# Kernel optimization log

Measured on AMD Instinct MI355X. Metric: run time of the kernel, lower is better.

## Reference

```python
import jax, jax.numpy as jnp
import numpy as np
import math

K_HEADS = 16  # nb_heads from init_kwargs


def setup_inputs() -> dict:
    key = jax.random.key(0)
    ks = jax.random.split(key, 7)
    B, M, H, D = 2, 2048, 1024, 1024 // K_HEADS
    return {
        "h": jax.random.normal(ks[0], (B, M, H), jnp.float32),
        "h_cache": jax.random.normal(ks[1], (B, M, H), jnp.float32),
        "key_pe": jax.random.normal(ks[2], (1, D, M), jnp.float32),
        "Wq": jax.random.normal(ks[3], (H, H), jnp.float32) * 0.02,
        "Wk": jax.random.normal(ks[4], (H, H), jnp.float32) * 0.02,
        "Wv": jax.random.normal(ks[5], (H, H), jnp.float32) * 0.02,
        "Wo": jax.random.normal(ks[6], (H, H), jnp.float32) * 0.02,
    }


def _heads(x, K):
    # [B, M, H] -> [B, K, M, D]
    B, M, H = x.shape
    return x.reshape(B, M, K, H // K).transpose(0, 2, 1, 3)


def reference(h, h_cache, key_pe, Wq, Wk, Wv, Wo):
    B, M, H = h.shape
    K = K_HEADS
    D = H // K
    q = _heads(h @ Wq.T, K)        # [B, K, M, D]
    k = _heads(h_cache @ Wk.T, K)  # [B, K, L, D], L == M
    v = _heads(h_cache @ Wv.T, K)  # [B, K, L, D]

    attn_cont = jnp.einsum("bkmd,bkld->bkml", q, k)            # content scores
    attn_pos = jnp.einsum("bkmd,dl->bkml", q, key_pe[0])       # positional scores
    attn = (attn_cont + attn_pos[..., :M]) / math.sqrt(D)
    attn = jax.nn.softmax(attn, axis=-1)  # computed as in source, but source
    # (faithfully) multiplies VALUE by attn_cont, not attn:
    out = jnp.einsum("bkml,bkld->bkmd", attn_cont, v)          # [B, K, M, D]
    out = out.transpose(0, 2, 1, 3).reshape(B, M, H)
    return out @ Wo.T
```

## Files before the change

kernel.cpp:

```cpp
#include <hip/hip_runtime.h>
#include <hip/hip_bf16.h>

#define BB 2
#define MM 2048
#define HH 1024
#define KH 16

typedef short s16x8 __attribute__((ext_vector_type(8)));
typedef float f32x4 __attribute__((ext_vector_type(4)));
typedef float f32x16 __attribute__((ext_vector_type(16)));

#define GLOBAL_AS __attribute__((address_space(1)))
#define LDS_AS    __attribute__((address_space(3)))

__device__ __forceinline__ void async_copy16(const void* g, void* l) {
    __builtin_amdgcn_global_load_lds((const GLOBAL_AS void*)g, (LDS_AS void*)l, 16, 0, 0);
}

struct __align__(8) bf16x4_t { __hip_bfloat16 x, y, z, w; };

__global__ __launch_bounds__(256) void cvt6b(
    const float* __restrict__ s0, const float* __restrict__ s1,
    const float* __restrict__ s2, const float* __restrict__ s3,
    const float* __restrict__ s4,
    __hip_bfloat16* __restrict__ d0, __hip_bfloat16* __restrict__ d1,
    __hip_bfloat16* __restrict__ d2, __hip_bfloat16* __restrict__ d3,
    __hip_bfloat16* __restrict__ d4,
    float* __restrict__ Sz)
{
    const int seg = blockIdx.y;
    const int i = (blockIdx.x * 256 + threadIdx.x) * 4;
    if (seg == 5) {
        if (i + 3 < BB * KH * 64 * 64) {
            float4 z = {0.f, 0.f, 0.f, 0.f};
            *(float4*)(Sz + i) = z;
        }
        return;
    }
    const float* src;
    __hip_bfloat16* dst;
    int n;
    switch (seg) {
        case 0: src = s0; dst = d0; n = BB * MM * HH; break;
        case 1: src = s1; dst = d1; n = BB * MM * HH; break;
        case 2: src = s2; dst = d2; n = HH * HH; break;
        case 3: src = s3; dst = d3; n = HH * HH; break;
        default: src = s4; dst = d4; n = HH * HH; break;
    }
    if (i + 3 < n) {
        const float4 v = *(const float4*)(src + i);
        bf16x4_t o;
        o.x = __float2bfloat16(v.x);
        o.y = __float2bfloat16(v.y);
        o.z = __float2bfloat16(v.z);
        o.w = __float2bfloat16(v.w);
        *(bf16x4_t*)(dst + i) = o;
    }
}

__global__ __launch_bounds__(256) void transpose_wq(
    const float* __restrict__ Wq, __hip_bfloat16* __restrict__ WqT)
{
    __shared__ float Tl[64][65];
    const int j0 = blockIdx.x * 64;
    const int k0 = blockIdx.y * 64;
    const int t = threadIdx.x;
    const int r = t >> 6;
    const int c = t & 63;
#pragma unroll
    for (int i = 0; i < 64; i += 4)
        Tl[r + i][c] = Wq[(size_t)(j0 + r + i) * HH + k0 + c];
    __syncthreads();
#pragma unroll
    for (int i = 0; i < 64; i += 4)
        WqT[(size_t)(k0 + r + i) * HH + j0 + c] = __float2bfloat16(Tl[c][r + i]);
}

__device__ __forceinline__ void store_c(__hip_bfloat16* C, size_t idx, float v) {
    C[idx] = __float2bfloat16(v);
}
__device__ __forceinline__ void store_c(float* C, size_t idx, float v) { C[idx] = v; }

template <typename OutT>
__device__ __forceinline__ void gemm_nt_body64(
    const __hip_bfloat16* __restrict__ A,
    const __hip_bfloat16* __restrict__ Bm,
    OutT* __restrict__ C,
    __hip_bfloat16* As, __hip_bfloat16* Bs,
    int m0, int n0)
{
    const int t    = threadIdx.x;
    const int lane = t & 63;
    const int wave = t >> 6;

    const int srow = lane >> 3;
    const int sw   = ((lane & 7) ^ srow) * 8;

    const int wm  = (wave >> 1) * 64;
    const int wn  = (wave & 1) * 64;
    const int fm  = lane & 31;
    const int fm7 = fm & 7;
    const int ghi = lane >> 5;

    f32x16 acc[2][2] = {};

    for (int k0 = 0; k0 < HH; k0 += 64) {
        __syncthreads();
#pragma unroll
        for (int i = 0; i < 2; ++i) {
            const int c = wave * 2 + i;
            const __hip_bfloat16* ag = A + (size_t)(m0 + c * 16 + srow) * HH + k0 + sw;
            async_copy16(ag,          As + c * 1024);
            async_copy16(ag + 8 * HH, As + c * 1024 + 512);
            const __hip_bfloat16* bg = Bm + (size_t)(n0 + c * 16 + srow) * HH + k0 + sw;
            async_copy16(bg,          Bs + c * 1024);
            async_copy16(bg + 8 * HH, Bs + c * 1024 + 512);
        }
        __syncthreads();

#pragma unroll
        for (int ks = 0; ks < 64; ks += 16) {
            const int pos = ((((ks >> 3) + ghi) ^ fm7) * 8);
            s16x8 af[2], bf[2];
#pragma unroll
            for (int mi = 0; mi < 2; ++mi)
                af[mi] = *(const s16x8*)(As + (wm + mi * 32 + fm) * 64 + pos);
#pragma unroll
            for (int ni = 0; ni < 2; ++ni)
                bf[ni] = *(const s16x8*)(Bs + (wn + ni * 32 + fm) * 64 + pos);
#pragma unroll
            for (int mi = 0; mi < 2; ++mi)
#pragma unroll
                for (int ni = 0; ni < 2; ++ni)
                    acc[mi][ni] = __builtin_amdgcn_mfma_f32_32x32x16_bf16(
                        af[mi], bf[ni], acc[mi][ni], 0, 0, 0);
        }
    }

    const int ec = lane & 31;
    const int eb = (lane >> 5) * 4;
#pragma unroll
    for (int mi = 0; mi < 2; ++mi)
#pragma unroll
        for (int ni = 0; ni < 2; ++ni)
#pragma unroll
            for (int r = 0; r < 16; ++r) {
                const int m = m0 + wm + mi * 32 + (r & 3) + 8 * (r >> 2) + eb;
                const int n = n0 + wn + ni * 32 + ec;
                store_c(C, (size_t)m * HH + n, acc[mi][ni][r]);
            }
}

template <typename OutT>
__device__ __forceinline__ void gemm_nt_body64_m64(
    const __hip_bfloat16* __restrict__ A,
    const __hip_bfloat16* __restrict__ Bm,
    OutT* __restrict__ C,
    __hip_bfloat16* As, __hip_bfloat16* Bs,
    int m0, int n0)
{
    const int t    = threadIdx.x;
    const int lane = t & 63;
    const int wave = t >> 6;

    const int srow = lane >> 3;
    const int sw   = ((lane & 7) ^ srow) * 8;

    const int wn  = wave * 32;
    const int fm  = lane & 31;
    const int fm7 = fm & 7;
    const int ghi = lane >> 5;

    f32x16 acc[2] = {};

    for (int k0 = 0; k0 < HH; k0 += 64) {
        __syncthreads();
        {
            const __hip_bfloat16* ag = A + (size_t)(m0 + wave * 16 + srow) * HH + k0 + sw;
            async_copy16(ag,          As + wave * 1024);
            async_copy16(ag + 8 * HH, As + wave * 1024 + 512);
        }
#pragma unroll
        for (int i = 0; i < 2; ++i) {
            const int c = wave * 2 + i;
            const __hip_bfloat16* bg = Bm + (size_t)(n0 + c * 16 + srow) * HH + k0 + sw;
            async_copy16(bg,          Bs + c * 1024);
            async_copy16(bg + 8 * HH, Bs + c * 1024 + 512);
        }
        __syncthreads();

#pragma unroll
        for (int ks = 0; ks < 64; ks += 16) {
            const int pos = ((((ks >> 3) + ghi) ^ fm7) * 8);
            s16x8 af[2], bf;
#pragma unroll
            for (int mi = 0; mi < 2; ++mi)
                af[mi] = *(const s16x8*)(As + (mi * 32 + fm) * 64 + pos);
            bf = *(const s16x8*)(Bs + (wn + fm) * 64 + pos);
#pragma unroll
            for (int mi = 0; mi < 2; ++mi)
                acc[mi] = __builtin_amdgcn_mfma_f32_32x32x16_bf16(
                    af[mi], bf, acc[mi], 0, 0, 0);
        }
    }

    const int ec = lane & 31;
    const int eb = (lane >> 5) * 4;
#pragma unroll
    for (int mi = 0; mi < 2; ++mi)
#pragma unroll
        for (int r = 0; r < 16; ++r) {
            const int m = m0 + mi * 32 + (r & 3) + 8 * (r >> 2) + eb;
            const int n = n0 + wn + ec;
            store_c(C, (size_t)m * HH + n, acc[mi][r]);
        }
}

__global__ __launch_bounds__(256) void gemm_kv(
    const __hip_bfloat16* __restrict__ hcb,
    const __hip_bfloat16* __restrict__ wk, const __hip_bfloat16* __restrict__ wv,
    __hip_bfloat16* __restrict__ K, __hip_bfloat16* __restrict__ V)
{
    __shared__ __align__(16) __hip_bfloat16 As[128 * 64];
    __shared__ __align__(16) __hip_bfloat16 Bs[128 * 64];
    const int z = blockIdx.z;
    gemm_nt_body64(hcb, z ? wv : wk, z ? V : K, As, Bs,
                   blockIdx.x * 128, blockIdx.y * 128);
}

__global__ __launch_bounds__(256) void gemm_f(
    const __hip_bfloat16* __restrict__ W2, const __hip_bfloat16* __restrict__ WqT,
    __hip_bfloat16* __restrict__ F)
{
    __shared__ __align__(16) __hip_bfloat16 As[64 * 64];
    __shared__ __align__(16) __hip_bfloat16 Bs[128 * 64];
    const int b = blockIdx.z;
    gemm_nt_body64_m64(W2 + (size_t)b * HH * HH, WqT, F + (size_t)b * HH * HH,
                       As, Bs, blockIdx.x * 64, blockIdx.y * 128);
}

__global__ __launch_bounds__(256) void gemm_final(
    const __hip_bfloat16* __restrict__ hb, const __hip_bfloat16* __restrict__ F,
    float* __restrict__ outg)
{
    __shared__ __align__(16) __hip_bfloat16 As[64 * 64];
    __shared__ __align__(16) __hip_bfloat16 Bs[128 * 64];
    const int b = blockIdx.z;
    gemm_nt_body64_m64(hb + (size_t)b * MM * HH, F + (size_t)b * HH * HH,
                       outg + (size_t)b * MM * HH, As, Bs,
                       blockIdx.x * 64, blockIdx.y * 128);
}

#define CH 128
#define LP 136

__global__ __launch_bounds__(256) void kv_outer_mfma(
    const __hip_bfloat16* __restrict__ Km,
    const __hip_bfloat16* __restrict__ Vm,
    float* __restrict__ S)
{
    __shared__ __align__(16) __hip_bfloat16 Kt[64 * LP];
    __shared__ __align__(16) __hip_bfloat16 Vt[64 * LP];

    const int t = threadIdx.x, head = blockIdx.y, b = blockIdx.z;
    const int l0 = blockIdx.x * CH;

    const int r  = t & 127;
    const int cb = (t >> 7) * 8;
    const size_t gbase = (size_t)(b * MM + l0 + r) * HH + head * 64;
#pragma unroll
    for (int u = 0; u < 4; ++u) {
        const int c8 = cb + u * 16;
        const s16x8 kv = *(const s16x8*)(Km + gbase + c8);
        const s16x8 vv = *(const s16x8*)(Vm + gbase + c8);
#pragma unroll
        for (int j = 0; j < 8; ++j) {
            Kt[(c8 + j) * LP + r] = ((const __hip_bfloat16*)&kv)[j];
            Vt[(c8 + j) * LP + r] = ((const __hip_bfloat16*)&vv)[j];
        }
    }
    __syncthreads();

    const int wave = t >> 6, lane = t & 63;
    const int fr = lane & 15;
    const int fq = (lane >> 4) * 8;
    const int wm = wave * 16;

    f32x4 acc[4] = {};
    for (int kk = 0; kk < CH; kk += 32) {
        const s16x8 af = *(const s16x8*)(Kt + (wm + fr) * LP + kk + fq);
        s16x8 bf[4];
#pragma unroll
        for (int nj = 0; nj < 4; ++nj)
            bf[nj] = *(const s16x8*)(Vt + (nj * 16 + fr) * LP + kk + fq);
#pragma unroll
        for (int nj = 0; nj < 4; ++nj)
            acc[nj] = __builtin_amdgcn_mfma_f32_16x16x32_bf16(af, bf[nj], acc[nj], 0, 0, 0);
    }

    float* Sg = S + ((size_t)b * KH + head) * 4096;
    const int er = (lane >> 4) * 4;
    const int ec = lane & 15;
#pragma unroll
    for (int nj = 0; nj < 4; ++nj)
#pragma unroll
        for (int rr = 0; rr < 4; ++rr)
            atomicAdd(&Sg[(wm + er + rr) * 64 + nj * 16 + ec], acc[nj][rr]);
}

__global__ __launch_bounds__(256) void w2_fold(
    const __hip_bfloat16* __restrict__ Wo,
    const float* __restrict__ S,
    __hip_bfloat16* __restrict__ W2)
{
    __shared__ float Sl[64 * 68];
    __shared__ float Wl[128 * 68];
    const int t = threadIdx.x, head = blockIdx.y, b = blockIdx.z;
    const int n0 = blockIdx.x * 128;

    const float* Sg = S + ((size_t)b * KH + head) * 4096;
    for (int idx = t; idx < 4096; idx += 256) {
        const int dp = idx >> 6, d = idx & 63;
        Sl[d * 68 + dp] = Sg[idx];
    }
    for (int idx = t; idx < 1024; idx += 256) {
        const int r = idx >> 3, c8 = (idx & 7) * 8;
        s16x8 wv = *(const s16x8*)(Wo + (size_t)(n0 + r) * HH + head * 64 + c8);
#pragma unroll
        for (int j = 0; j < 8; ++j) {
            __hip_bfloat16 wb = *(((const __hip_bfloat16*)&wv) + j);
            Wl[r * 68 + c8 + j] = __bfloat162float(wb);
        }
    }
    __syncthreads();

    const int dpb = (t & 15) * 4;
    const int ng  = t >> 4;
    float acc[8][4] = {};
    for (int d0 = 0; d0 < 64; d0 += 4) {
        f32x4 sv[4];
#pragma unroll
        for (int r = 0; r < 4; ++r)
            sv[r] = *(const f32x4*)(Sl + (d0 + r) * 68 + dpb);
#pragma unroll
        for (int i = 0; i < 8; ++i) {
            const f32x4 wv = *(const f32x4*)(Wl + (ng + 16 * i) * 68 + d0);
#pragma unroll
            for (int r = 0; r < 4; ++r)
#pragma unroll
                for (int j = 0; j < 4; ++j)
                    acc[i][j] += wv[r] * sv[r][j];
        }
    }

#pragma unroll
    for (int i = 0; i < 8; ++i) {
        bf16x4_t o;
        o.x = __float2bfloat16(acc[i][0]);
        o.y = __float2bfloat16(acc[i][1]);
        o.z = __float2bfloat16(acc[i][2]);
        o.w = __float2bfloat16(acc[i][3]);
        *(bf16x4_t*)(W2 + (size_t)b * HH * HH + (size_t)(n0 + ng + 16 * i) * HH
                     + head * 64 + dpb) = o;
    }
}

extern "C" void kernel_launch(void* const* d_in, const int* in_sizes, int n_in,
                              void* d_out, int out_size, void* d_ws, size_t ws_size,
                              hipStream_t stream) {
    const float* h_f  = (const float*)d_in[0];
    const float* hc_f = (const float*)d_in[1];
    const float* Wq_f = (const float*)d_in[3];
    const float* Wk_f = (const float*)d_in[4];
    const float* Wv_f = (const float*)d_in[5];
    const float* Wo_f = (const float*)d_in[6];
    float* out = (float*)d_out;

    const size_t act_b = (size_t)BB * MM * HH * 2;
    const size_t w_b   = (size_t)HH * HH * 2;
    char* ws = (char*)d_ws;
    __hip_bfloat16* hb   = (__hip_bfloat16*)(ws);
    __hip_bfloat16* hcb  = (__hip_bfloat16*)(ws + act_b);
    __hip_bfloat16* wkb  = (__hip_bfloat16*)(ws + 2 * act_b);
    __hip_bfloat16* wvb  = (__hip_bfloat16*)(ws + 2 * act_b + w_b);
    __hip_bfloat16* wob  = (__hip_bfloat16*)(ws + 2 * act_b + 2 * w_b);
    __hip_bfloat16* wqt  = (__hip_bfloat16*)(ws + 2 * act_b + 3 * w_b);
    __hip_bfloat16* Kbuf = (__hip_bfloat16*)(ws + 2 * act_b + 4 * w_b);
    __hip_bfloat16* Vbuf = (__hip_bfloat16*)(ws + 3 * act_b + 4 * w_b);
    float*          Sbuf = (float*)(ws + 4 * act_b + 4 * w_b);
    __hip_bfloat16* W2   = (__hip_bfloat16*)(ws + 4 * act_b + 4 * w_b + (size_t)512 * 1024);
    __hip_bfloat16* Fbuf = (__hip_bfloat16*)(ws + 4 * act_b + 6 * w_b + (size_t)512 * 1024);

    const dim3 blk(256);

    cvt6b<<<dim3(4096, 6), blk, 0, stream>>>(h_f, hc_f, Wk_f, Wv_f, Wo_f,
                                             hb, hcb, wkb, wvb, wob, Sbuf);
    transpose_wq<<<dim3(16, 16), blk, 0, stream>>>(Wq_f, wqt);

    gemm_kv<<<dim3(32, 8, 2), blk, 0, stream>>>(hcb, wkb, wvb, Kbuf, Vbuf);

    kv_outer_mfma<<<dim3(MM / CH, KH, BB), blk, 0, stream>>>(Kbuf, Vbuf, Sbuf);

    w2_fold<<<dim3(8, KH, BB), blk, 0, stream>>>(wob, Sbuf, W2);

    gemm_f<<<dim3(16, 8, 2), blk, 0, stream>>>(W2, wqt, Fbuf);

    gemm_final<<<dim3(32, 8, 2), blk, 0, stream>>>(hb, Fbuf, out);
}
```

Measured before the change: 174.1 us.

## Fuse K/V projection GEMM with per-head K^T V outer product

Replaces the separate K/V projection GEMM and the K^T·V reduction kernel with one kernel. Each block computes a 128-row by 64-column (one head) tile of both K and V, stages it in LDS as bf16, and immediately accumulates K^T V into S with atomics. This drops the global write and re-read of the full K and V activations and one launch. In exchange each block reloads the same h_cache tile per head, and the grid shrinks to 512 blocks with smaller N tiles.

```diff
diff --git a/kernel.cpp b/kernel.cpp
--- a/kernel.cpp
+++ b/kernel.cpp
@@ -81,74 +81,123 @@
 }
 __device__ __forceinline__ void store_c(float* C, size_t idx, float v) { C[idx] = v; }
 
-template <typename OutT>
-__device__ __forceinline__ void gemm_nt_body64(
-    const __hip_bfloat16* __restrict__ A,
-    const __hip_bfloat16* __restrict__ Bm,
-    OutT* __restrict__ C,
-    __hip_bfloat16* As, __hip_bfloat16* Bs,
-    int m0, int n0)
-{
+#define LP2 136
+
+__global__ __launch_bounds__(256) void gemm_kvt(
+    const __hip_bfloat16* __restrict__ hcb,
+    const __hip_bfloat16* __restrict__ wk, const __hip_bfloat16* __restrict__ wv,
+    float* __restrict__ S)
+{
+    __shared__ __align__(16) char smem[64 * LP2 * 2 * 2];
+    __hip_bfloat16* As  = (__hip_bfloat16*)smem;
+    __hip_bfloat16* Bsk = (__hip_bfloat16*)(smem + 16384);
+    __hip_bfloat16* Bsv = (__hip_bfloat16*)(smem + 24576);
+    __hip_bfloat16* Kt  = (__hip_bfloat16*)smem;
+    __hip_bfloat16* Vt  = (__hip_bfloat16*)(smem + 64 * LP2 * 2);
+
     const int t    = threadIdx.x;
     const int lane = t & 63;
     const int wave = t >> 6;
+    const int head = blockIdx.y;
+    const int m0   = blockIdx.x * 128;
+    const int n0   = head * 64;
+    const int b    = blockIdx.x >> 4;
 
     const int srow = lane >> 3;
     const int sw   = ((lane & 7) ^ srow) * 8;
 
     const int wm  = (wave >> 1) * 64;
-    const int wn  = (wave & 1) * 64;
+    const int wn  = (wave & 1) * 32;
     const int fm  = lane & 31;
     const int fm7 = fm & 7;
     const int ghi = lane >> 5;
 
-    f32x16 acc[2][2] = {};
+    f32x16 acck[2] = {};
+    f32x16 accv[2] = {};
 
     for (int k0 = 0; k0 < HH; k0 += 64) {
         __syncthreads();
 #pragma unroll
+        for (int i = 0; i < 4; ++i) {
+            const int c = wave * 4 + i;
+            async_copy16(hcb + (size_t)(m0 + c * 8 + srow) * HH + k0 + sw,
+                         As + c * 512);
+        }
+#pragma unroll
         for (int i = 0; i < 2; ++i) {
             const int c = wave * 2 + i;
-            const __hip_bfloat16* ag = A + (size_t)(m0 + c * 16 + srow) * HH + k0 + sw;
-            async_copy16(ag,          As + c * 1024);
-            async_copy16(ag + 8 * HH, As + c * 1024 + 512);
-            const __hip_bfloat16* bg = Bm + (size_t)(n0 + c * 16 + srow) * HH + k0 + sw;
-            async_copy16(bg,          Bs + c * 1024);
-            async_copy16(bg + 8 * HH, Bs + c * 1024 + 512);
+            async_copy16(wk + (size_t)(n0 + c * 8 + srow) * HH + k0 + sw,
+                         Bsk + c * 512);
+            async_copy16(wv + (size_t)(n0 + c * 8 + srow) * HH + k0 + sw,
+                         Bsv + c * 512);
         }
         __syncthreads();
 
 #pragma unroll
         for (int ks = 0; ks < 64; ks += 16) {
             const int pos = ((((ks >> 3) + ghi) ^ fm7) * 8);
-            s16x8 af[2], bf[2];
+            s16x8 af[2];
 #pragma unroll
             for (int mi = 0; mi < 2; ++mi)
                 af[mi] = *(const s16x8*)(As + (wm + mi * 32 + fm) * 64 + pos);
-#pragma unroll
-            for (int ni = 0; ni < 2; ++ni)
-                bf[ni] = *(const s16x8*)(Bs + (wn + ni * 32 + fm) * 64 + pos);
-#pragma unroll
-            for (int mi = 0; mi < 2; ++mi)
-#pragma unroll
-                for (int ni = 0; ni < 2; ++ni)
-                    acc[mi][ni] = __builtin_amdgcn_mfma_f32_32x32x16_bf16(
-                        af[mi], bf[ni], acc[mi][ni], 0, 0, 0);
-        }
-    }
-
-    const int ec = lane & 31;
-    const int eb = (lane >> 5) * 4;
+            const s16x8 bk = *(const s16x8*)(Bsk + (wn + fm) * 64 + pos);
+            const s16x8 bv = *(const s16x8*)(Bsv + (wn + fm) * 64 + pos);
+#pragma unroll
+            for (int mi = 0; mi < 2; ++mi) {
+                acck[mi] = __builtin_amdgcn_mfma_f32_32x32x16_bf16(af[mi], bk, acck[mi], 0, 0, 0);
+                accv[mi] = __builtin_amdgcn_mfma_f32_32x32x16_bf16(af[mi], bv, accv[mi], 0, 0, 0);
+            }
+        }
+    }
+
+    __syncthreads();
+
+    const int dcol = wn + (lane & 31);
+    const int lhi  = 4 * (lane >> 5);
 #pragma unroll
     for (int mi = 0; mi < 2; ++mi)
 #pragma unroll
-        for (int ni = 0; ni < 2; ++ni)
-#pragma unroll
-            for (int r = 0; r < 16; ++r) {
-                const int m = m0 + wm + mi * 32 + (r & 3) + 8 * (r >> 2) + eb;
-                const int n = n0 + wn + ni * 32 + ec;
-                store_c(C, (size_t)m * HH + n, acc[mi][ni][r]);
-            }
+        for (int g = 0; g < 4; ++g) {
+            const int lb = wm + mi * 32 + 8 * g + lhi;
+            bf16x4_t ok, ov;
+            ok.x = __float2bfloat16(acck[mi][4 * g + 0]);
+            ok.y = __float2bfloat16(acck[mi][4 * g + 1]);
+            ok.z = __float2bfloat16(acck[mi][4 * g + 2]);
+            ok.w = __float2bfloat16(acck[mi][4 * g + 3]);
+            ov.x = __float2bfloat16(accv[mi][4 * g + 0]);
+            ov.y = __float2bfloat16(accv[mi][4 * g + 1]);
+            ov.z = __float2bfloat16(accv[mi][4 * g + 2]);
+            ov.w = __float2bfloat16(accv[mi][4 * g + 3]);
+            *(bf16x4_t*)(Kt + dcol * LP2 + lb) = ok;
+            *(bf16x4_t*)(Vt + dcol * LP2 + lb) = ov;
+        }
+    __syncthreads();
+
+    const int fr = lane & 15;
+    const int fq = (lane >> 4) * 8;
+    const int wm2 = wave * 16;
+
+    f32x4 acc2[4] = {};
+#pragma unroll
+    for (int kk = 0; kk < 128; kk += 32) {
+        const s16x8 af = *(const s16x8*)(Kt + (wm2 + fr) * LP2 + kk + fq);
+        s16x8 bf[4];
+#pragma unroll
+        for (int nj = 0; nj < 4; ++nj)
+            bf[nj] = *(const s16x8*)(Vt + (nj * 16 + fr) * LP2 + kk + fq);
+#pragma unroll
+        for (int nj = 0; nj < 4; ++nj)
+            acc2[nj] = __builtin_amdgcn_mfma_f32_16x16x32_bf16(af, bf[nj], acc2[nj], 0, 0, 0);
+    }
+
+    float* Sg = S + ((size_t)b * KH + head) * 4096;
+    const int er = (lane >> 4) * 4;
+    const int ec = lane & 15;
+#pragma unroll
+    for (int nj = 0; nj < 4; ++nj)
+#pragma unroll
+        for (int rr = 0; rr < 4; ++rr)
+            atomicAdd(&Sg[(wm2 + er + rr) * 64 + nj * 16 + ec], acc2[nj][rr]);
 }
 
 template <typename OutT>
@@ -216,18 +265,6 @@
         }
 }
 
-__global__ __launch_bounds__(256) void gemm_kv(
-    const __hip_bfloat16* __restrict__ hcb,
-    const __hip_bfloat16* __restrict__ wk, const __hip_bfloat16* __restrict__ wv,
-    __hip_bfloat16* __restrict__ K, __hip_bfloat16* __restrict__ V)
-{
-    __shared__ __align__(16) __hip_bfloat16 As[128 * 64];
-    __shared__ __align__(16) __hip_bfloat16 Bs[128 * 64];
-    const int z = blockIdx.z;
-    gemm_nt_body64(hcb, z ? wv : wk, z ? V : K, As, Bs,
-                   blockIdx.x * 128, blockIdx.y * 128);
-}
-
 __global__ __launch_bounds__(256) void gemm_f(
     const __hip_bfloat16* __restrict__ W2, const __hip_bfloat16* __restrict__ WqT,
     __hip_bfloat16* __restrict__ F)
@@ -249,63 +286,6 @@
     gemm_nt_body64_m64(hb + (size_t)b * MM * HH, F + (size_t)b * HH * HH,
                        outg + (size_t)b * MM * HH, As, Bs,
                        blockIdx.x * 64, blockIdx.y * 128);
-}
-
-#define CH 128
-#define LP 136
-
-__global__ __launch_bounds__(256) void kv_outer_mfma(
-    const __hip_bfloat16* __restrict__ Km,
-    const __hip_bfloat16* __restrict__ Vm,
-    float* __restrict__ S)
-{
-    __shared__ __align__(16) __hip_bfloat16 Kt[64 * LP];
-    __shared__ __align__(16) __hip_bfloat16 Vt[64 * LP];
-
-    const int t = threadIdx.x, head = blockIdx.y, b = blockIdx.z;
-    const int l0 = blockIdx.x * CH;
-
-    const int r  = t & 127;
-    const int cb = (t >> 7) * 8;
-    const size_t gbase = (size_t)(b * MM + l0 + r) * HH + head * 64;
-#pragma unroll
-    for (int u = 0; u < 4; ++u) {
-        const int c8 = cb + u * 16;
-        const s16x8 kv = *(const s16x8*)(Km + gbase + c8);
-        const s16x8 vv = *(const s16x8*)(Vm + gbase + c8);
-#pragma unroll
-        for (int j = 0; j < 8; ++j) {
-            Kt[(c8 + j) * LP + r] = ((const __hip_bfloat16*)&kv)[j];
-            Vt[(c8 + j) * LP + r] = ((const __hip_bfloat16*)&vv)[j];
-        }
-    }
-    __syncthreads();
-
-    const int wave = t >> 6, lane = t & 63;
-    const int fr = lane & 15;
-    const int fq = (lane >> 4) * 8;
-    const int wm = wave * 16;
-
-    f32x4 acc[4] = {};
-    for (int kk = 0; kk < CH; kk += 32) {
-        const s16x8 af = *(const s16x8*)(Kt + (wm + fr) * LP + kk + fq);
-        s16x8 bf[4];
-#pragma unroll
-        for (int nj = 0; nj < 4; ++nj)
-            bf[nj] = *(const s16x8*)(Vt + (nj * 16 + fr) * LP + kk + fq);
-#pragma unroll
-        for (int nj = 0; nj < 4; ++nj)
-            acc[nj] = __builtin_amdgcn_mfma_f32_16x16x32_bf16(af, bf[nj], acc[nj], 0, 0, 0);
-    }
-
-    float* Sg = S + ((size_t)b * KH + head) * 4096;
-    const int er = (lane >> 4) * 4;
-    const int ec = lane & 15;
-#pragma unroll
-    for (int nj = 0; nj < 4; ++nj)
-#pragma unroll
-        for (int rr = 0; rr < 4; ++rr)
-            atomicAdd(&Sg[(wm + er + rr) * 64 + nj * 16 + ec], acc[nj][rr]);
 }
 
 __global__ __launch_bounds__(256) void w2_fold(
@@ -385,11 +365,9 @@
     __hip_bfloat16* wvb  = (__hip_bfloat16*)(ws + 2 * act_b + w_b);
     __hip_bfloat16* wob  = (__hip_bfloat16*)(ws + 2 * act_b + 2 * w_b);
     __hip_bfloat16* wqt  = (__hip_bfloat16*)(ws + 2 * act_b + 3 * w_b);
-    __hip_bfloat16* Kbuf = (__hip_bfloat16*)(ws + 2 * act_b + 4 * w_b);
-    __hip_bfloat16* Vbuf = (__hip_bfloat16*)(ws + 3 * act_b + 4 * w_b);
-    float*          Sbuf = (float*)(ws + 4 * act_b + 4 * w_b);
-    __hip_bfloat16* W2   = (__hip_bfloat16*)(ws + 4 * act_b + 4 * w_b + (size_t)512 * 1024);
-    __hip_bfloat16* Fbuf = (__hip_bfloat16*)(ws + 4 * act_b + 6 * w_b + (size_t)512 * 1024);
+    float*          Sbuf = (float*)(ws + 2 * act_b + 4 * w_b);
+    __hip_bfloat16* W2   = (__hip_bfloat16*)(ws + 2 * act_b + 4 * w_b + (size_t)512 * 1024);
+    __hip_bfloat16* Fbuf = (__hip_bfloat16*)(ws + 2 * act_b + 6 * w_b + (size_t)512 * 1024);
 
     const dim3 blk(256);
 
@@ -397,9 +375,7 @@
                                              hb, hcb, wkb, wvb, wob, Sbuf);
     transpose_wq<<<dim3(16, 16), blk, 0, stream>>>(Wq_f, wqt);
 
-    gemm_kv<<<dim3(32, 8, 2), blk, 0, stream>>>(hcb, wkb, wvb, Kbuf, Vbuf);
-
-    kv_outer_mfma<<<dim3(MM / CH, KH, BB), blk, 0, stream>>>(Kbuf, Vbuf, Sbuf);
+    gemm_kvt<<<dim3(32, KH), blk, 0, stream>>>(hcb, wkb, wvb, Sbuf);
 
     w2_fold<<<dim3(8, KH, BB), blk, 0, stream>>>(wob, Sbuf, W2);
 
```

Result: faster. 166.7 us (-4.2%).
